# Kernel tuning notes

Measured on AMD Instinct MI355X. Metric: run time of the kernel, lower is better.

## Reference

```python
import jax, jax.numpy as jnp
import numpy as np

N, D, L = 4096, 256, 3
E = 1.0  # eye scale 'e'


def _adj(X, W, b):
    # AdjLearner_intra: two Linear+ELU layers, then dense similarity h @ h.T -> [N, N]
    h = jax.nn.elu(X @ W[0] + b[0])
    h = jax.nn.elu(h @ W[1] + b[1])
    return h @ h.T


def _mlp(x, W, b, bn):
    # GIN MLP: Linear -> BatchNorm1d (batch stats, training mode) -> ReLU -> Linear
    h = x @ W[0] + b[0]
    mu = h.mean(axis=0)
    var = h.var(axis=0)  # biased, matches torch BN training normalization
    h = (h - mu) * jax.lax.rsqrt(var + 1e-5) * bn[0] + bn[1]
    return jax.nn.relu(h) @ W[1] + b[1]


def _gin(X, aW, ab, mW, mb, mbn):
    I = jnp.eye(X.shape[0], dtype=X.dtype)
    acc = jnp.zeros_like(X)
    for i in range(L):  # fixed small layer count
        adj = _adj(X, aW, ab)
        oh = (adj > adj.mean()).astype(X.dtype)  # adj_onehot: threshold at global mean
        X = _mlp((oh + E * I) @ X, mW[i], mb[i], mbn[i])
        acc = acc + X
    return acc / L


def setup_inputs() -> dict:
    key = jax.random.key(0)
    ks = jax.random.split(key, 16)
    s = np.float32(1.0 / np.sqrt(D))
    d = {}
    for i, name in enumerate(["QV", "Q", "V", "A"]):
        d[name] = jax.random.normal(ks[i], (N, D), jnp.float32)
    for j, br in enumerate(["qv", "t", "v"]):
        k0, k1 = ks[4 + 2 * j], ks[5 + 2 * j]
        d[f"adjW_{br}"] = jax.random.normal(k0, (2, D, D), jnp.float32) * s
        d[f"adjb_{br}"] = jnp.zeros((2, D), jnp.float32)
        d[f"mlpW_{br}"] = jax.random.normal(k1, (L, 2, D, D), jnp.float32) * s
        d[f"mlpb_{br}"] = jnp.zeros((L, 2, D), jnp.float32)
        d[f"mlpbn_{br}"] = jnp.stack(
            [jnp.ones((L, D), jnp.float32), jnp.zeros((L, D), jnp.float32)], axis=1
        )  # [L, 2(gamma,beta), D]
    return d


def reference(QV, Q, V, A,
              adjW_qv, adjb_qv, mlpW_qv, mlpb_qv, mlpbn_qv,
              adjW_t, adjb_t, mlpW_t, mlpb_t, mlpbn_t,
              adjW_v, adjb_v, mlpW_v, mlpb_v, mlpbn_v):
    GQV = _gin(QV, adjW_qv, adjb_qv, mlpW_qv, mlpb_qv, mlpbn_qv)  # type=1
    GQ = _gin(Q, adjW_t, adjb_t, mlpW_t, mlpb_t, mlpbn_t)          # type=2
    GV = _gin(V, adjW_v, adjb_v, mlpW_v, mlpb_v, mlpbn_v)          # type=3
    GA = _gin(A, adjW_t, adjb_t, mlpW_t, mlpb_t, mlpbn_t)          # type=2 (shared with Q branch)
    mse = lambda a, b: jnp.mean((a - b) ** 2)
    return (mse(GQV, GA), mse(GQ, GA), mse(GV, GA))
```

## Files before the change

kernel.cpp:

```cpp
#include <hip/hip_runtime.h>
#include <hip/hip_bf16.h>
#include <stdint.h>

#define NN 4096
#define DD 256
#define NL 3
typedef unsigned int uint;
typedef unsigned short ushort_t;

typedef float f32x4 __attribute__((ext_vector_type(4)));
typedef short bf16x8 __attribute__((ext_vector_type(8)));

struct Ptrs4 { const float* p0; const float* p1; const float* p2; const float* p3; };
__device__ __forceinline__ const float* sel(const Ptrs4& p, int b) {
    return b == 0 ? p.p0 : b == 1 ? p.p1 : b == 2 ? p.p2 : p.p3;
}

__device__ __forceinline__ uint pkbf2(float a, float b) {
    __hip_bfloat162 t = __float22bfloat162_rn(float2{a, b});
    union { __hip_bfloat162 h; uint u; } c; c.h = t; return c.u;
}
__device__ __forceinline__ void split3_pk(float a, float b, uint& h, uint& m, uint& l) {
    h = pkbf2(a, b);
    float ha = __uint_as_float(h << 16), hb = __uint_as_float(h & 0xFFFF0000u);
    float ra = a - ha, rb = b - hb;
    m = pkbf2(ra, rb);
    float ma = __uint_as_float(m << 16), mb = __uint_as_float(m & 0xFFFF0000u);
    l = pkbf2(ra - ma, rb - mb);
}

typedef __attribute__((address_space(3))) uint lds_u32;
typedef __attribute__((address_space(1))) const uint glb_u32;
__device__ __forceinline__ void gload16(void* l, const void* g) {
    __builtin_amdgcn_global_load_lds((glb_u32*)g, (lds_u32*)l, 16, 0, 0);
}
__device__ __forceinline__ void gload4(void* l, const void* g) {
    __builtin_amdgcn_global_load_lds((glb_u32*)g, (lds_u32*)l, 4, 0, 0);
}

template<int MODE>
__global__ __launch_bounds__(256, 4)
void gemm_small(const float* __restrict__ Xin, Ptrs4 Wp, Ptrs4 bp,
                float* __restrict__ Out, float* __restrict__ cs, float* __restrict__ csq,
                ushort_t* __restrict__ Hso)
{
    const int b = blockIdx.z;
    const float* Wb = sel(Wp, b);
    const float* bb = sel(bp, b);
    const float* X = Xin + (size_t)b * NN * DD;
    float* O = Out + (size_t)b * NN * DD;
    ushort_t* HsO = Hso + (size_t)b * 3 * (size_t)DD * NN;
    const int row0 = blockIdx.y * 128, col0 = blockIdx.x * 64;
    const int tid = threadIdx.x;
    __shared__ float Asm[16][132];
    __shared__ float Bsm[16][68];
    const int tr = (tid >> 4) << 3, tc = (tid & 15) << 2;
    const int m = tid & 127, kk = (tid >> 7) << 3;
    const int bk = tid >> 4, bn = (tid & 15) << 2;
    const float* aSrc = X + (size_t)(row0 + m) * DD + kk;
    const float* bSrc = Wb + (size_t)bk * DD + col0 + bn;

    float acc[8][4] = {};
    float4 pa0 = *(const float4*)(aSrc);
    float4 pa1 = *(const float4*)(aSrc + 4);
    float4 pb  = *(const float4*)(bSrc);
    for (int t = 0; t < DD / 16; ++t) {
        Asm[kk+0][m]=pa0.x; Asm[kk+1][m]=pa0.y; Asm[kk+2][m]=pa0.z; Asm[kk+3][m]=pa0.w;
        Asm[kk+4][m]=pa1.x; Asm[kk+5][m]=pa1.y; Asm[kk+6][m]=pa1.z; Asm[kk+7][m]=pa1.w;
        *(float4*)&Bsm[bk][bn] = pb;
        __syncthreads();
        if (t < DD / 16 - 1) {
            const int k0 = (t + 1) * 16;
            pa0 = *(const float4*)(aSrc + k0);
            pa1 = *(const float4*)(aSrc + k0 + 4);
            pb  = *(const float4*)(bSrc + (size_t)k0 * DD);
        }
        #pragma unroll
        for (int k = 0; k < 16; ++k) {
            float a[8], bv[4];
            *(float4*)&a[0] = *(const float4*)&Asm[k][tr];
            *(float4*)&a[4] = *(const float4*)&Asm[k][tr + 4];
            *(float4*)&bv[0] = *(const float4*)&Bsm[k][tc];
            #pragma unroll
            for (int i = 0; i < 8; ++i)
                #pragma unroll
                for (int j = 0; j < 4; ++j)
                    acc[i][j] = fmaf(a[i], bv[j], acc[i][j]);
        }
        __syncthreads();
    }
    float bias4[4];
    *(float4*)bias4 = *(const float4*)(bb + col0 + tc);
    float s4[4] = {0.f,0.f,0.f,0.f}, q4[4] = {0.f,0.f,0.f,0.f};
    const int dph = col0 + tc;
    const size_t sb3 = (size_t)(dph >> 3) * (NN * 8) + (dph & 4);
    #pragma unroll
    for (int i = 0; i < 8; ++i) {
        float ov[4];
        #pragma unroll
        for (int j = 0; j < 4; ++j) {
            float v = acc[i][j] + bias4[j];
            if (MODE == 0 || MODE == 1 || MODE == 3) v = (v > 0.f) ? v : (expf(v) - 1.f);
            ov[j] = v;
            if (MODE == 1 || MODE == 3) s4[j] += v;
            if (MODE == 2) { s4[j] += v; q4[j] += v * v; }
        }
        if (MODE == 3) {
            uint2 vh, vm, vl;
            split3_pk(ov[0], ov[1], vh.x, vm.x, vl.x);
            split3_pk(ov[2], ov[3], vh.y, vm.y, vl.y);
            size_t off = sb3 + (size_t)(row0 + tr + i) * 8;
            *(uint2*)(HsO + off) = vh;
            *(uint2*)(HsO + (size_t)DD * NN + off) = vm;
            *(uint2*)(HsO + (size_t)2 * DD * NN + off) = vl;
        } else {
            float4 o; o.x = ov[0]; o.y = ov[1]; o.z = ov[2]; o.w = ov[3];
            *(float4*)(O + (size_t)(row0 + tr + i) * DD + col0 + tc) = o;
        }
    }
    if (MODE == 1 || MODE == 2 || MODE == 3) {
        __syncthreads();
        const int rg = tid >> 4;
        #pragma unroll
        for (int j = 0; j < 4; ++j) {
            Asm[rg][tc + j] = s4[j];
            if (MODE == 2) Bsm[rg][tc + j] = q4[j];
        }
        __syncthreads();
        if (tid < 64) {
            float s = 0.f, q = 0.f;
            #pragma unroll
            for (int r = 0; r < 16; ++r) { s += Asm[r][tid]; if (MODE == 2) q += Bsm[r][tid]; }
            atomicAdd(&cs[b * DD + col0 + tid], s);
            if (MODE == 2) atomicAdd(&csq[b * DD + col0 + tid], q);
        }
    }
}

__global__ void thresh_k(const float* __restrict__ cs, float* __restrict__ tvals)
{
    const int b = blockIdx.x, t = threadIdx.x;
    __shared__ float red[256];
    float v = cs[b * DD + t];
    red[t] = v * v;
    __syncthreads();
    for (int s = 128; s > 0; s >>= 1) { if (t < s) red[t] += red[t + s]; __syncthreads(); }
    if (t == 0) tvals[b] = red[0] * (1.0f / 16777216.0f);
}

__global__ __launch_bounds__(256)
void tsplit_x(const float* __restrict__ Xin, ushort_t* __restrict__ Sh,
              ushort_t* __restrict__ Sm, ushort_t* __restrict__ Sl)
{
    const int b = blockIdx.z;
    const int n0 = blockIdx.x * 64, d0 = blockIdx.y * 64;
    const float* X = Xin + (size_t)b * NN * DD;
    __shared__ float ls[64][65];
    const int tid = threadIdx.x;
    #pragma unroll
    for (int i = 0; i < 4; ++i) {
        int u = (i << 8) + tid;
        int r = u >> 4, c4 = (u & 15) << 2;
        float4 v = *(const float4*)(X + (size_t)(n0 + r) * DD + d0 + c4);
        ls[r][c4] = v.x; ls[r][c4+1] = v.y; ls[r][c4+2] = v.z; ls[r][c4+3] = v.w;
    }
    __syncthreads();
    const int d = tid >> 2, seg = (tid & 3) << 4;
    uint ph[8], pm[8], pl[8];
    #pragma unroll
    for (int jj = 0; jj < 8; ++jj) {
        float a = ls[seg + 2 * jj][d];
        float c = ls[seg + 2 * jj + 1][d];
        split3_pk(a, c, ph[jj], pm[jj], pl[jj]);
    }
    size_t idx = ((size_t)(b * DD + d0 + d)) * NN + n0 + seg;
    *(uint4*)(Sh + idx)     = *(uint4*)&ph[0];
    *(uint4*)(Sh + idx + 8) = *(uint4*)&ph[4];
    *(uint4*)(Sm + idx)     = *(uint4*)&pm[0];
    *(uint4*)(Sm + idx + 8) = *(uint4*)&pm[4];
    *(uint4*)(Sl + idx)     = *(uint4*)&pl[0];
    *(uint4*)(Sl + idx + 8) = *(uint4*)&pl[4];
}

__global__ __launch_bounds__(256, 3)
void adj_mfma_s(const float* __restrict__ H, const float* __restrict__ tvals,
                uint8_t* __restrict__ mask)
{
    int t = blockIdx.x;
    int by = 0, rem = 32;
    while (t >= rem) { t -= rem; rem--; by++; }
    const int bx = by + t;
    const int b = blockIdx.z;
    const int row0 = by * 128, col0 = bx * 128;
    const int tid = threadIdx.x;
    const int wave = tid >> 6, ln = tid & 15, quad = (tid >> 4) & 3;
    const int wrow = wave >> 1, wcol = wave & 1;
    const float* Hb = H + (size_t)b * NN * DD;
    uint8_t* Mb = mask + (size_t)b * NN * (NN / 8);
    __shared__ ushort_t hs[2][3][128][34];

    f32x4 acc[4][4] = {};
    for (int k0 = 0; k0 < DD; k0 += 32) {
        #pragma unroll
        for (int i = 0; i < 8; ++i) {
            int f = (i << 8) + tid;
            int sr = f >> 3;
            int side = sr >> 7, r = sr & 127, part = f & 7;
            int grow = (side ? col0 : row0) + r;
            float4 v = *(const float4*)(Hb + (size_t)grow * DD + k0 + part * 4);
            uint h0, m0, l0, h1, m1, l1;
            split3_pk(v.x, v.y, h0, m0, l0);
            split3_pk(v.z, v.w, h1, m1, l1);
            uint2 ph; ph.x = h0; ph.y = h1;
            uint2 pm; pm.x = m0; pm.y = m1;
            uint2 pl; pl.x = l0; pl.y = l1;
            *(uint2*)&hs[side][0][r][part * 4] = ph;
            *(uint2*)&hs[side][1][r][part * 4] = pm;
            *(uint2*)&hs[side][2][r][part * 4] = pl;
        }
        __syncthreads();
        bf16x8 af[4][3];
        #pragma unroll
        for (int mt = 0; mt < 4; ++mt)
            #pragma unroll
            for (int lvl = 0; lvl < 3; ++lvl)
                af[mt][lvl] = *(const bf16x8*)&hs[0][lvl][wrow * 64 + mt * 16 + ln][quad * 8];
        #pragma unroll
        for (int nt = 0; nt < 4; ++nt) {
            int n = wcol * 64 + nt * 16 + ln;
            bf16x8 bh = *(const bf16x8*)&hs[1][0][n][quad * 8];
            bf16x8 bm = *(const bf16x8*)&hs[1][1][n][quad * 8];
            bf16x8 bl = *(const bf16x8*)&hs[1][2][n][quad * 8];
            #pragma unroll
            for (int mt = 0; mt < 4; ++mt) {
                f32x4 a = acc[mt][nt];
                a = __builtin_amdgcn_mfma_f32_16x16x32_bf16(af[mt][0], bh, a, 0, 0, 0);
                a = __builtin_amdgcn_mfma_f32_16x16x32_bf16(af[mt][0], bm, a, 0, 0, 0);
                a = __builtin_amdgcn_mfma_f32_16x16x32_bf16(af[mt][1], bh, a, 0, 0, 0);
                a = __builtin_amdgcn_mfma_f32_16x16x32_bf16(af[mt][0], bl, a, 0, 0, 0);
                a = __builtin_amdgcn_mfma_f32_16x16x32_bf16(af[mt][2], bh, a, 0, 0, 0);
                a = __builtin_amdgcn_mfma_f32_16x16x32_bf16(af[mt][1], bm, a, 0, 0, 0);
                acc[mt][nt] = a;
            }
        }
        __syncthreads();
    }
    const float t2 = tvals[b];
    #pragma unroll
    for (int mt = 0; mt < 4; ++mt)
        #pragma unroll
        for (int nt = 0; nt < 4; ++nt) {
            bool p0 = acc[mt][nt][0] > t2, p1 = acc[mt][nt][1] > t2;
            bool p2 = acc[mt][nt][2] > t2, p3 = acc[mt][nt][3] > t2;
            unsigned long long bal[4];
            bal[0] = __ballot(p0); bal[1] = __ballot(p1);
            bal[2] = __ballot(p2); bal[3] = __ballot(p3);
            if ((tid & 63) < 16) {
                int q = ln >> 2, rsel = ln & 3;
                unsigned long long bv = rsel == 0 ? bal[0] : rsel == 1 ? bal[1]
                                       : rsel == 2 ? bal[2] : bal[3];
                ushort_t u16 = (ushort_t)((bv >> (q * 16)) & 0xFFFFull);
                int row = row0 + wrow * 64 + mt * 16 + ln;
                int colb = (col0 + wcol * 64 + nt * 16) >> 3;
                *(ushort_t*)(Mb + (size_t)row * (NN / 8) + colb) = u16;
            }
            uint nib = (p0 ? 1u : 0u) | (p1 ? 2u : 0u) | (p2 ? 4u : 0u) | (p3 ? 8u : 0u);
            uint other = (uint)__shfl_xor((int)nib, 16);
            if ((quad & 1) == 0) {
                uint byt = nib | (other << 4);
                int rowm = col0 + wcol * 64 + nt * 16 + ln;
                int colbm = ((row0 + wrow * 64 + mt * 16) >> 3) + (quad >> 1);
                Mb[(size_t)rowm * (NN / 8) + colbm] = (uint8_t)byt;
            }
        }
}

__global__ __launch_bounds__(256, 3)
void adj_mfma_v2(const ushort_t* __restrict__ Hs, const float* __restrict__ tvals,
                 uint8_t* __restrict__ mask)
{
    int t = blockIdx.x;
    int by = 0, rem = 32;
    while (t >= rem) { t -= rem; rem--; by++; }
    const int bx = by + t;
    const int b = blockIdx.z;
    const int row0 = by * 128, col0 = bx * 128;
    const int tid = threadIdx.x;
    const int wave = tid >> 6, ln = tid & 15, quad = (tid >> 4) & 3;
    const int wrow = wave >> 1, wcol = wave & 1;
    const ushort_t* Hb = Hs + (size_t)b * 3 * (size_t)DD * NN;
    uint8_t* Mb = mask + (size_t)b * NN * (NN / 8);
    __shared__ ushort_t hs2[6][4][128][8];

    const int grow = tid & 127;
    const int qb = tid >> 7;
    const size_t var0 = (size_t)qb * (NN * 8) + (size_t)(row0 + grow) * 8;
    const size_t var1 = (size_t)qb * (NN * 8) + (size_t)(col0 + grow) * 8;

    f32x4 acc[4][4] = {};
    for (int kb0 = 0; kb0 < DD / 8; kb0 += 4) {
        #pragma unroll
        for (int c = 0; c < 12; ++c) {
            const int sl = c >> 1, part = c & 1;
            const int side = sl / 3, lvl = sl % 3;
            const ushort_t* g = Hb + (size_t)lvl * DD * NN
                                   + (size_t)(kb0 + part * 2) * (NN * 8)
                                   + (side ? var1 : var0);
            char* l = (char*)&hs2[0][0][0][0] + (((sl * 8 + part * 4 + wave)) << 10);
            gload16(l, g);
        }
        __syncthreads();
        bf16x8 af[4][3];
        #pragma unroll
        for (int mt = 0; mt < 4; ++mt)
            #pragma unroll
            for (int lvl = 0; lvl < 3; ++lvl)
                af[mt][lvl] = *(const bf16x8*)&hs2[lvl][quad][wrow * 64 + mt * 16 + ln][0];
        #pragma unroll
        for (int nt = 0; nt < 4; ++nt) {
            const int n = wcol * 64 + nt * 16 + ln;
            bf16x8 bh = *(const bf16x8*)&hs2[3][quad][n][0];
            bf16x8 bm = *(const bf16x8*)&hs2[4][quad][n][0];
            bf16x8 bl = *(const bf16x8*)&hs2[5][quad][n][0];
            #pragma unroll
            for (int mt = 0; mt < 4; ++mt) {
                f32x4 a = acc[mt][nt];
                a = __builtin_amdgcn_mfma_f32_16x16x32_bf16(af[mt][0], bh, a, 0, 0, 0);
                a = __builtin_amdgcn_mfma_f32_16x16x32_bf16(af[mt][0], bm, a, 0, 0, 0);
                a = __builtin_amdgcn_mfma_f32_16x16x32_bf16(af[mt][1], bh, a, 0, 0, 0);
                a = __builtin_amdgcn_mfma_f32_16x16x32_bf16(af[mt][0], bl, a, 0, 0, 0);
                a = __builtin_amdgcn_mfma_f32_16x16x32_bf16(af[mt][2], bh, a, 0, 0, 0);
                a = __builtin_amdgcn_mfma_f32_16x16x32_bf16(af[mt][1], bm, a, 0, 0, 0);
                acc[mt][nt] = a;
            }
        }
        __syncthreads();
    }
    const float t2 = tvals[b];
    #pragma unroll
    for (int mt = 0; mt < 4; ++mt)
        #pragma unroll
        for (int nt = 0; nt < 4; ++nt) {
            bool p0 = acc[mt][nt][0] > t2, p1 = acc[mt][nt][1] > t2;
            bool p2 = acc[mt][nt][2] > t2, p3 = acc[mt][nt][3] > t2;
            unsigned long long bal[4];
            bal[0] = __ballot(p0); bal[1] = __ballot(p1);
            bal[2] = __ballot(p2); bal[3] = __ballot(p3);
            if ((tid & 63) < 16) {
                int q = ln >> 2, rsel = ln & 3;
                unsigned long long bv = rsel == 0 ? bal[0] : rsel == 1 ? bal[1]
                                       : rsel == 2 ? bal[2] : bal[3];
                ushort_t u16 = (ushort_t)((bv >> (q * 16)) & 0xFFFFull);
                int row = row0 + wrow * 64 + mt * 16 + ln;
                int colb = (col0 + wcol * 64 + nt * 16) >> 3;
                *(ushort_t*)(Mb + (size_t)row * (NN / 8) + colb) = u16;
            }
            uint nib = (p0 ? 1u : 0u) | (p1 ? 2u : 0u) | (p2 ? 4u : 0u) | (p3 ? 8u : 0u);
            uint other = (uint)__shfl_xor((int)nib, 16);
            if ((quad & 1) == 0) {
                uint byt = nib | (other << 4);
                int rowm = col0 + wcol * 64 + nt * 16 + ln;
                int colbm = ((row0 + wrow * 64 + mt * 16) >> 3) + (quad >> 1);
                Mb[(size_t)rowm * (NN / 8) + colbm] = (uint8_t)byt;
            }
        }
}

__global__ __launch_bounds__(256)
void masked_mfma(float* __restrict__ Xio, const ushort_t* __restrict__ Sh,
                 const ushort_t* __restrict__ Sm, const ushort_t* __restrict__ Sl,
                 const uint8_t* __restrict__ mask)
{
    const int b = blockIdx.z;
    const int row0 = blockIdx.y * 128, col0 = blockIdx.x * 64;
    const int tid = threadIdx.x;
    const int wave = tid >> 6, ln = tid & 15, quad = (tid >> 4) & 3;
    const int wrow = wave >> 1, wcol = wave & 1;
    float* X = Xio + (size_t)b * NN * DD;
    const size_t sb = (size_t)b * DD * NN;
    const ushort_t* Ss[3] = { Sh + sb, Sm + sb, Sl + sb };
    const uint* Mw = (const uint*)(mask + (size_t)b * NN * (NN / 8));
    __shared__ ushort_t bt2[2][3][2][64][32];
    __shared__ uint msk2[2][2][128];
    __shared__ uint lut[256][4];

    #pragma unroll
    for (int p = 0; p < 4; ++p)
        lut[tid][p] = (((tid >> (2 * p)) & 1u) ? 0x3F80u : 0u) |
                      (((tid >> (2 * p + 1)) & 1u) ? 0x3F800000u : 0u);

    const int c = tid >> 2;
    const int qp = (tid & 3) ^ ((tid >> 3) & 3);
    const size_t goff = (size_t)(col0 + c) * NN + (size_t)qp * 8;
    const size_t mrow = (size_t)(row0 + (tid & 127)) * 128;

    f32x4 acc[4][2] = {};

    #define STAGE(buf, t)                                                         \
        {                                                                         \
            const size_t j_ = (size_t)(t) * 64;                                   \
            _Pragma("unroll")                                                     \
            for (int lvl = 0; lvl < 3; ++lvl) {                                   \
                gload16((char*)&bt2[buf][lvl][0][0][0] + (wave << 10),            \
                        Ss[lvl] + goff + j_);                                     \
                gload16((char*)&bt2[buf][lvl][1][0][0] + (wave << 10),            \
                        Ss[lvl] + goff + j_ + 32);                                \
            }                                                                     \
            if (tid < 128) {                                                      \
                gload4((char*)&msk2[buf][0][0] + (wave << 8), Mw + mrow + 2*(t)); \
                gload4((char*)&msk2[buf][1][0] + (wave << 8), Mw + mrow + 2*(t)+1);\
            }                                                                     \
        }

    STAGE(0, 0);
    __syncthreads();

    for (int t = 0; t < NN / 64; ++t) {
        const int cur = t & 1;
        if (t < NN / 64 - 1) STAGE(cur ^ 1, t + 1);
        #pragma unroll
        for (int kk = 0; kk < 2; ++kk) {
            bf16x8 afr[4];
            #pragma unroll
            for (int mt = 0; mt < 4; ++mt) {
                uint w = msk2[cur][kk][wrow * 64 + mt * 16 + ln];
                uint byte = (w >> (quad * 8)) & 0xFFu;
                afr[mt] = *(const bf16x8*)&lut[byte][0];
            }
            #pragma unroll
            for (int nt = 0; nt < 2; ++nt) {
                const int n = wcol * 32 + nt * 16 + ln;
                const int slot = (quad ^ ((n >> 1) & 3)) * 8;
                bf16x8 bh = *(const bf16x8*)&bt2[cur][0][kk][n][slot];
                bf16x8 bm = *(const bf16x8*)&bt2[cur][1][kk][n][slot];
                bf16x8 bl = *(const bf16x8*)&bt2[cur][2][kk][n][slot];
                #pragma unroll
                for (int mt = 0; mt < 4; ++mt) {
                    f32x4 a = acc[mt][nt];
                    a = __builtin_amdgcn_mfma_f32_16x16x32_bf16(afr[mt], bh, a, 0, 0, 0);
                    a = __builtin_amdgcn_mfma_f32_16x16x32_bf16(afr[mt], bm, a, 0, 0, 0);
                    a = __builtin_amdgcn_mfma_f32_16x16x32_bf16(afr[mt], bl, a, 0, 0, 0);
                    acc[mt][nt] = a;
                }
            }
        }
        __syncthreads();
    }
    #undef STAGE
    #pragma unroll
    for (int mt = 0; mt < 4; ++mt)
        #pragma unroll
        for (int nt = 0; nt < 2; ++nt)
            #pragma unroll
            for (int r = 0; r < 4; ++r) {
                int row = row0 + wrow * 64 + mt * 16 + quad * 4 + r;
                int col = col0 + wcol * 32 + nt * 16 + ln;
                size_t idx = (size_t)row * DD + col;
                X[idx] = X[idx] + acc[mt][nt][r];
            }
}

__global__ __launch_bounds__(256, 4)
void gemm_bnrelu(const float* __restrict__ G, Ptrs4 Wp, Ptrs4 bp, Ptrs4 gbp,
                 const float* __restrict__ bns, const float* __restrict__ bnq,
                 float* __restrict__ Xout, float* __restrict__ accb, int first)
{
    const int b = blockIdx.z;
    const float* Wb = sel(Wp, b);
    const float* bb = sel(bp, b);
    const float* gb = sel(gbp, b);
    const float* Gb = G + (size_t)b * NN * DD;
    float* O = Xout + (size_t)b * NN * DD;
    float* Ab = accb + (size_t)b * NN * DD;
    const int row0 = blockIdx.y * 128, col0 = blockIdx.x * 64;
    const int tid = threadIdx.x;
    __shared__ float Asm[16][132];
    __shared__ float Bsm[16][68];
    __shared__ float scs[DD], shs[DD];
    {
        float mu = bns[b * DD + tid] * (1.0f / NN);
        float ms = bnq[b * DD + tid] * (1.0f / NN);
        float var = ms - mu * mu;
        float sc = gb[tid] / sqrtf(var + 1e-5f);
        scs[tid] = sc;
        shs[tid] = gb[DD + tid] - mu * sc;
    }
    __syncthreads();
    const int tr = (tid >> 4) << 3, tc = (tid & 15) << 2;
    const int m = tid & 127, kk = (tid >> 7) << 3;
    const int bk = tid >> 4, bn = (tid & 15) << 2;
    const float* aSrc = Gb + (size_t)(row0 + m) * DD + kk;
    const float* bSrc = Wb + (size_t)bk * DD + col0 + bn;

    float acc[8][4] = {};
    float4 pa0 = *(const float4*)(aSrc);
    float4 pa1 = *(const float4*)(aSrc + 4);
    float4 pb  = *(const float4*)(bSrc);
    for (int t = 0; t < DD / 16; ++t) {
        {
            const int kg = t * 16 + kk;
            float vv[8] = {pa0.x, pa0.y, pa0.z, pa0.w, pa1.x, pa1.y, pa1.z, pa1.w};
            #pragma unroll
            for (int i = 0; i < 8; ++i) {
                float v = fmaf(vv[i], scs[kg + i], shs[kg + i]);
                Asm[kk + i][m] = v > 0.f ? v : 0.f;
            }
            *(float4*)&Bsm[bk][bn] = pb;
        }
        __syncthreads();
        if (t < DD / 16 - 1) {
            const int k0 = (t + 1) * 16;
            pa0 = *(const float4*)(aSrc + k0);
            pa1 = *(const float4*)(aSrc + k0 + 4);
            pb  = *(const float4*)(bSrc + (size_t)k0 * DD);
        }
        #pragma unroll
        for (int k = 0; k < 16; ++k) {
            float a[8], bv[4];
            *(float4*)&a[0] = *(const float4*)&Asm[k][tr];
            *(float4*)&a[4] = *(const float4*)&Asm[k][tr + 4];
            *(float4*)&bv[0] = *(const float4*)&Bsm[k][tc];
            #pragma unroll
            for (int i = 0; i < 8; ++i)
                #pragma unroll
                for (int j = 0; j < 4; ++j)
                    acc[i][j] = fmaf(a[i], bv[j], acc[i][j]);
        }
        __syncthreads();
    }
    float bias4[4];
    *(float4*)bias4 = *(const float4*)(bb + col0 + tc);
    #pragma unroll
    for (int i = 0; i < 8; ++i) {
        size_t idx = (size_t)(row0 + tr + i) * DD + col0 + tc;
        float4 o;
        o.x = acc[i][0] + bias4[0]; o.y = acc[i][1] + bias4[1];
        o.z = acc[i][2] + bias4[2]; o.w = acc[i][3] + bias4[3];
        *(float4*)(O + idx) = o;
        if (first) {
            *(float4*)(Ab + idx) = o;
        } else {
            float4 p = *(const float4*)(Ab + idx);
            p.x += o.x; p.y += o.y; p.z += o.z; p.w += o.w;
            *(float4*)(Ab + idx) = p;
        }
    }
}

__global__ __launch_bounds__(256)
void mse_partial(const float* __restrict__ accb, double* __restrict__ msep)
{
    const int pair = blockIdx.x;
    const float* A_ = accb + (size_t)pair * NN * DD;
    const float* B_ = accb + (size_t)3 * NN * DD;
    const size_t total = (size_t)NN * DD;
    double s = 0.0;
    for (size_t i = (size_t)blockIdx.y * blockDim.x + threadIdx.x; i < total;
         i += (size_t)gridDim.y * blockDim.x) {
        float d = A_[i] - B_[i];
        s += (double)d * (double)d;
    }
    __shared__ double red[256];
    red[threadIdx.x] = s;
    __syncthreads();
    for (int st = 128; st > 0; st >>= 1) {
        if (threadIdx.x < st) red[threadIdx.x] += red[threadIdx.x + st];
        __syncthreads();
    }
    if (threadIdx.x == 0) atomicAdd(&msep[pair], red[0]);
}

__global__ void mse_final(const double* __restrict__ msep, float* __restrict__ out)
{
    int i = threadIdx.x;
    if (i < 3) out[i] = (float)(msep[i] / ((double)NN * DD) / 9.0);
}

static inline Ptrs4 mk4(const float* a, const float* b, const float* c, const float* d) {
    Ptrs4 p; p.p0 = a; p.p1 = b; p.p2 = c; p.p3 = d; return p;
}

extern "C" void kernel_launch(void* const* d_in, const int* in_sizes, int n_in,
                              void* d_out, int out_size, void* d_ws, size_t ws_size,
                              hipStream_t stream)
{
    (void)in_sizes; (void)n_in; (void)out_size;
    const float* adjW[3]  = {(const float*)d_in[4],  (const float*)d_in[9],  (const float*)d_in[14]};
    const float* adjb[3]  = {(const float*)d_in[5],  (const float*)d_in[10], (const float*)d_in[15]};
    const float* mlpW[3]  = {(const float*)d_in[6],  (const float*)d_in[11], (const float*)d_in[16]};
    const float* mlpb[3]  = {(const float*)d_in[7],  (const float*)d_in[12], (const float*)d_in[17]};
    const float* mlpbn[3] = {(const float*)d_in[8],  (const float*)d_in[13], (const float*)d_in[18]};

    char* ws = (char*)d_ws;
    double* msep  = (double*)ws;
    float* colsum = (float*)(ws + 64);
    float* bnsum  = colsum + 3 * 4 * DD;
    float* bnsq   = bnsum  + 3 * 4 * DD;
    float* tvals  = bnsq   + 3 * 4 * DD;
    const size_t tensN = (size_t)4 * NN * DD;
    const size_t HS_BYTES = (size_t)4 * 3 * DD * NN * 2;
    const size_t MASK_BYTES = (size_t)4 * NN * (NN / 8);

    float* Xbuf = (float*)(ws + 65536);
    float* Abuf = Xbuf + tensN;

    const size_t need_fast = 65536 + 2 * tensN * 4 + HS_BYTES + tensN * 4 + MASK_BYTES;
    const bool fast = ws_size >= need_fast;

    float* Bbuf = nullptr; float* accb; uint8_t* mask;
    ushort_t *Sh, *Sm, *Sl, *HsG = nullptr;
    if (fast) {
        char* hr = (char*)(Abuf + tensN);
        HsG  = (ushort_t*)hr;
        Sl   = (ushort_t*)hr;
        accb = (float*)(hr + HS_BYTES);
        mask = (uint8_t*)(accb + tensN);
    } else {
        Bbuf = Abuf + tensN;
        accb = Bbuf + tensN;
        mask = (uint8_t*)(accb + tensN);
        Sl   = (ushort_t*)Bbuf;
    }
    Sh = (ushort_t*)Abuf;
    Sm = Sh + tensN;

    hipMemsetAsync(ws, 0, 64 + 3 * 3 * 4 * DD * sizeof(float), stream);
    for (int b = 0; b < 4; ++b)
        hipMemcpyAsync(Xbuf + (size_t)b * NN * DD, d_in[b], (size_t)NN * DD * sizeof(float),
                       hipMemcpyDeviceToDevice, stream);

    dim3 gS(4, 32, 4);
    dim3 gA(528, 1, 4);
    dim3 gT(64, 4, 4);
    dim3 blk(256);

    for (int l = 0; l < NL; ++l) {
        float* cs_l = colsum + l * 4 * DD;
        float* bs_l = bnsum + l * 4 * DD;
        float* bq_l = bnsq  + l * 4 * DD;
        #define MK(arr, off) mk4(arr[0] + (off), arr[1] + (off), arr[2] + (off), arr[1] + (off))
        gemm_small<0><<<gS, blk, 0, stream>>>(Xbuf, MK(adjW, 0), MK(adjb, 0), Abuf,
                                              nullptr, nullptr, (ushort_t*)nullptr);
        if (fast) {
            gemm_small<3><<<gS, blk, 0, stream>>>(Abuf, MK(adjW, (size_t)DD * DD), MK(adjb, DD),
                                                  nullptr, cs_l, nullptr, HsG);
            thresh_k<<<4, blk, 0, stream>>>(cs_l, tvals);
            adj_mfma_v2<<<gA, blk, 0, stream>>>(HsG, tvals, mask);
        } else {
            gemm_small<1><<<gS, blk, 0, stream>>>(Abuf, MK(adjW, (size_t)DD * DD), MK(adjb, DD),
                                                  Bbuf, cs_l, nullptr, (ushort_t*)nullptr);
            thresh_k<<<4, blk, 0, stream>>>(cs_l, tvals);
            adj_mfma_s<<<gA, blk, 0, stream>>>(Bbuf, tvals, mask);
        }
        tsplit_x<<<gT, blk, 0, stream>>>(Xbuf, Sh, Sm, Sl);
        masked_mfma<<<gS, blk, 0, stream>>>(Xbuf, Sh, Sm, Sl, mask);
        const size_t w0 = (size_t)l * 2 * DD * DD, b0 = (size_t)l * 2 * DD;
        gemm_small<2><<<gS, blk, 0, stream>>>(Xbuf, MK(mlpW, w0), MK(mlpb, b0), Abuf,
                                              bs_l, bq_l, (ushort_t*)nullptr);
        gemm_bnrelu<<<gS, blk, 0, stream>>>(Abuf, MK(mlpW, w0 + (size_t)DD * DD), MK(mlpb, b0 + DD),
                                            MK(mlpbn, b0), bs_l, bq_l, Xbuf, accb, (l == 0) ? 1 : 0);
        #undef MK
    }
    mse_partial<<<dim3(3, 64), blk, 0, stream>>>(accb, msep);
    mse_final<<<1, 64, 0, stream>>>(msep, (float*)d_out);
}
```

Baseline: 1.164 ms.

## Run the small feature GEMMs on MFMA with a 3-way bf16 split of pre-split weights

Adds a one-time kernel that splits every adjacency and MLP weight matrix into transposed hi/mid/lo bf16 planes in workspace. Adds MFMA-based replacements for the first adjacency linear, the first MLP linear (with BN statistics) and the BN+ReLU second linear. These split activations on the fly and emulate fp32 accuracy with six bf16 MFMAs per tile. The goal is to move these DxD GEMMs off the fp32 vector ALU; the cost is extra split work, extra workspace, and a dependence on workspace being large enough.

```diff
diff --git a/kernel.cpp b/kernel.cpp
--- a/kernel.cpp
+++ b/kernel.cpp
@@ -15,6 +15,12 @@
 __device__ __forceinline__ const float* sel(const Ptrs4& p, int b) {
     return b == 0 ? p.p0 : b == 1 ? p.p1 : b == 2 ? p.p2 : p.p3;
 }
+struct Ptrs4U { const ushort_t* p0; const ushort_t* p1; const ushort_t* p2; const ushort_t* p3; };
+__device__ __forceinline__ const ushort_t* selU(const Ptrs4U& p, int b) {
+    return b == 0 ? p.p0 : b == 1 ? p.p1 : b == 2 ? p.p2 : p.p3;
+}
+struct PtrsW { const float* a0; const float* a1; const float* a2;
+               const float* m0; const float* m1; const float* m2; };
 
 __device__ __forceinline__ uint pkbf2(float a, float b) {
     __hip_bfloat162 t = __float22bfloat162_rn(float2{a, b});
@@ -135,6 +141,308 @@
             if (MODE == 2) atomicAdd(&csq[b * DD + col0 + tid], q);
         }
     }
+}
+
+__global__ __launch_bounds__(256)
+void wsplitk(PtrsW W, ushort_t* __restrict__ Wsp)
+{
+    const int z = blockIdx.z;
+    const float* src;
+    if (z < 6) {
+        const float* base = (z >> 1) == 0 ? W.a0 : (z >> 1) == 1 ? W.a1 : W.a2;
+        src = base + (size_t)(z & 1) * DD * DD;
+    } else {
+        int zz = z - 6;
+        const float* base = (zz / 6) == 0 ? W.m0 : (zz / 6) == 1 ? W.m1 : W.m2;
+        src = base + (size_t)(zz % 6) * DD * DD;
+    }
+    ushort_t* dst = Wsp + (size_t)z * 3 * DD * DD;
+    const int k0 = blockIdx.x * 64, c0 = blockIdx.y * 64;
+    __shared__ float ls[64][65];
+    const int tid = threadIdx.x;
+    #pragma unroll
+    for (int i = 0; i < 4; ++i) {
+        int u = (i << 8) + tid;
+        int r = u >> 4, c4 = (u & 15) << 2;
+        float4 v = *(const float4*)(src + (size_t)(k0 + r) * DD + c0 + c4);
+        ls[r][c4] = v.x; ls[r][c4+1] = v.y; ls[r][c4+2] = v.z; ls[r][c4+3] = v.w;
+    }
+    __syncthreads();
+    const int col = tid >> 2, seg = (tid & 3) << 4;
+    uint ph[8], pm[8], pl[8];
+    #pragma unroll
+    for (int jj = 0; jj < 8; ++jj) {
+        float a = ls[seg + 2 * jj][col];
+        float c = ls[seg + 2 * jj + 1][col];
+        split3_pk(a, c, ph[jj], pm[jj], pl[jj]);
+    }
+    size_t idx = (size_t)(c0 + col) * DD + k0 + seg;
+    #pragma unroll
+    for (int lvl = 0; lvl < 3; ++lvl) {
+        uint* pp = lvl == 0 ? ph : lvl == 1 ? pm : pl;
+        *(uint4*)(dst + (size_t)lvl * DD * DD + idx)     = *(uint4*)&pp[0];
+        *(uint4*)(dst + (size_t)lvl * DD * DD + idx + 8) = *(uint4*)&pp[4];
+    }
+}
+
+template<int MODE>
+__global__ void gemm_mfma(const float* __restrict__ Xin, Ptrs4U Wsp, Ptrs4 bp,
+                          float* __restrict__ Out, float* __restrict__ cs,
+                          float* __restrict__ csq)
+{
+    const int b = blockIdx.z;
+    const ushort_t* Wb = selU(Wsp, b);
+    const float* bb = sel(bp, b);
+    const float* X = Xin + (size_t)b * NN * DD;
+    float* O = Out + (size_t)b * NN * DD;
+    const int row0 = blockIdx.y * 128, col0 = blockIdx.x * 64;
+    const int tid = threadIdx.x;
+    const int wave = tid >> 6, ln = tid & 15, quad = (tid >> 4) & 3;
+    const int wrow = wave >> 1, wcol = wave & 1;
+    __shared__ ushort_t As[3][128][32];
+    __shared__ ushort_t Bs[2][3][64][32];
+
+    const int arow = tid >> 1, kb16 = (tid & 1) << 4;
+    const int xr = (arow >> 1) & 3;
+    const int s0 = (((kb16 >> 3) + 0) ^ xr) << 3;
+    const int s1 = (((kb16 >> 3) + 1) ^ xr) << 3;
+    const float* aSrc = X + (size_t)(row0 + arow) * DD + kb16;
+
+    const int qp = (tid & 3) ^ ((tid >> 3) & 3);
+    const size_t bgoff = (size_t)(col0 + (tid >> 2)) * DD + (size_t)qp * 8;
+
+    #define BSTAGE(buf, t_) { \
+        _Pragma("unroll") \
+        for (int lvl = 0; lvl < 3; ++lvl) \
+            gload16((char*)&Bs[buf][lvl][0][0] + (wave << 10), \
+                    Wb + (size_t)lvl * DD * DD + bgoff + (size_t)(t_) * 32); }
+
+    f32x4 acc[4][2] = {};
+    float4 pa0 = *(const float4*)(aSrc),     pa1 = *(const float4*)(aSrc + 4);
+    float4 pa2 = *(const float4*)(aSrc + 8), pa3 = *(const float4*)(aSrc + 12);
+    BSTAGE(0, 0)
+    for (int t = 0; t < DD / 32; ++t) {
+        {
+            uint hh[8], mm[8], ll[8];
+            split3_pk(pa0.x, pa0.y, hh[0], mm[0], ll[0]);
+            split3_pk(pa0.z, pa0.w, hh[1], mm[1], ll[1]);
+            split3_pk(pa1.x, pa1.y, hh[2], mm[2], ll[2]);
+            split3_pk(pa1.z, pa1.w, hh[3], mm[3], ll[3]);
+            split3_pk(pa2.x, pa2.y, hh[4], mm[4], ll[4]);
+            split3_pk(pa2.z, pa2.w, hh[5], mm[5], ll[5]);
+            split3_pk(pa3.x, pa3.y, hh[6], mm[6], ll[6]);
+            split3_pk(pa3.z, pa3.w, hh[7], mm[7], ll[7]);
+            uint4 v;
+            v.x=hh[0]; v.y=hh[1]; v.z=hh[2]; v.w=hh[3]; *(uint4*)&As[0][arow][s0] = v;
+            v.x=hh[4]; v.y=hh[5]; v.z=hh[6]; v.w=hh[7]; *(uint4*)&As[0][arow][s1] = v;
+            v.x=mm[0]; v.y=mm[1]; v.z=mm[2]; v.w=mm[3]; *(uint4*)&As[1][arow][s0] = v;
+            v.x=mm[4]; v.y=mm[5]; v.z=mm[6]; v.w=mm[7]; *(uint4*)&As[1][arow][s1] = v;
+            v.x=ll[0]; v.y=ll[1]; v.z=ll[2]; v.w=ll[3]; *(uint4*)&As[2][arow][s0] = v;
+            v.x=ll[4]; v.y=ll[5]; v.z=ll[6]; v.w=ll[7]; *(uint4*)&As[2][arow][s1] = v;
+        }
+        __syncthreads();
+        if (t < DD / 32 - 1) {
+            const float* an = aSrc + (t + 1) * 32;
+            pa0 = *(const float4*)(an);     pa1 = *(const float4*)(an + 4);
+            pa2 = *(const float4*)(an + 8); pa3 = *(const float4*)(an + 12);
+            BSTAGE((t + 1) & 1, t + 1)
+        }
+        bf16x8 af[4][3];
+        #pragma unroll
+        for (int mt = 0; mt < 4; ++mt) {
+            const int row = wrow * 64 + mt * 16 + ln;
+            const int sl = ((quad ^ ((row >> 1) & 3)) << 3);
+            #pragma unroll
+            for (int lvl = 0; lvl < 3; ++lvl)
+                af[mt][lvl] = *(const bf16x8*)&As[lvl][row][sl];
+        }
+        const int cur = t & 1;
+        #pragma unroll
+        for (int nt = 0; nt < 2; ++nt) {
+            const int n = wcol * 32 + nt * 16 + ln;
+            const int slot = ((quad ^ ((n >> 1) & 3)) << 3);
+            bf16x8 bh = *(const bf16x8*)&Bs[cur][0][n][slot];
+            bf16x8 bm = *(const bf16x8*)&Bs[cur][1][n][slot];
+            bf16x8 bl = *(const bf16x8*)&Bs[cur][2][n][slot];
+            #pragma unroll
+            for (int mt = 0; mt < 4; ++mt) {
+                f32x4 a = acc[mt][nt];
+                a = __builtin_amdgcn_mfma_f32_16x16x32_bf16(af[mt][0], bh, a, 0, 0, 0);
+                a = __builtin_amdgcn_mfma_f32_16x16x32_bf16(af[mt][0], bm, a, 0, 0, 0);
+                a = __builtin_amdgcn_mfma_f32_16x16x32_bf16(af[mt][1], bh, a, 0, 0, 0);
+                a = __builtin_amdgcn_mfma_f32_16x16x32_bf16(af[mt][0], bl, a, 0, 0, 0);
+                a = __builtin_amdgcn_mfma_f32_16x16x32_bf16(af[mt][2], bh, a, 0, 0, 0);
+                a = __builtin_amdgcn_mfma_f32_16x16x32_bf16(af[mt][1], bm, a, 0, 0, 0);
+                acc[mt][nt] = a;
+            }
+        }
+        __syncthreads();
+    }
+    #undef BSTAGE
+
+    float bcol[2], ssum[2] = {0.f, 0.f}, qsum[2] = {0.f, 0.f};
+    #pragma unroll
+    for (int nt = 0; nt < 2; ++nt) bcol[nt] = bb[col0 + wcol * 32 + nt * 16 + ln];
+    #pragma unroll
+    for (int mt = 0; mt < 4; ++mt)
+        #pragma unroll
+        for (int nt = 0; nt < 2; ++nt)
+            #pragma unroll
+            for (int r = 0; r < 4; ++r) {
+                int row = row0 + wrow * 64 + mt * 16 + quad * 4 + r;
+                int col = col0 + wcol * 32 + nt * 16 + ln;
+                float v = acc[mt][nt][r] + bcol[nt];
+                if (MODE == 0) v = (v > 0.f) ? v : (expf(v) - 1.f);
+                if (MODE == 2) { ssum[nt] += v; qsum[nt] += v * v; }
+                O[(size_t)row * DD + col] = v;
+            }
+    if (MODE == 2) {
+        float* scrS = (float*)&As[0][0][0];
+        float* scrQ = scrS + 512;
+        const int rg = wrow * 4 + quad;
+        #pragma unroll
+        for (int nt = 0; nt < 2; ++nt) {
+            const int cl = wcol * 32 + nt * 16 + ln;
+            scrS[rg * 64 + cl] = ssum[nt];
+            scrQ[rg * 64 + cl] = qsum[nt];
+        }
+        __syncthreads();
+        if (tid < 64) {
+            float s = 0.f, q = 0.f;
+            #pragma unroll
+            for (int r = 0; r < 8; ++r) { s += scrS[r * 64 + tid]; q += scrQ[r * 64 + tid]; }
+            atomicAdd(&cs[b * DD + col0 + tid], s);
+            atomicAdd(&csq[b * DD + col0 + tid], q);
+        }
+    }
+}
+
+__global__ void gemm_bnrelu_m(const float* __restrict__ G, Ptrs4U Wsp, Ptrs4 bp, Ptrs4 gbp,
+                              const float* __restrict__ bns, const float* __restrict__ bnq,
+                              float* __restrict__ Xout, float* __restrict__ accb, int first)
+{
+    const int b = blockIdx.z;
+    const ushort_t* Wb = selU(Wsp, b);
+    const float* bb = sel(bp, b);
+    const float* gb = sel(gbp, b);
+    const float* Gb = G + (size_t)b * NN * DD;
+    float* O = Xout + (size_t)b * NN * DD;
+    float* Ab = accb + (size_t)b * NN * DD;
+    const int row0 = blockIdx.y * 128, col0 = blockIdx.x * 64;
+    const int tid = threadIdx.x;
+    const int wave = tid >> 6, ln = tid & 15, quad = (tid >> 4) & 3;
+    const int wrow = wave >> 1, wcol = wave & 1;
+    __shared__ ushort_t As[3][128][32];
+    __shared__ ushort_t Bs[2][3][64][32];
+    __shared__ float scs[DD], shs[DD];
+    {
+        float mu = bns[b * DD + tid] * (1.0f / NN);
+        float ms = bnq[b * DD + tid] * (1.0f / NN);
+        float var = ms - mu * mu;
+        float sc = gb[tid] / sqrtf(var + 1e-5f);
+        scs[tid] = sc;
+        shs[tid] = gb[DD + tid] - mu * sc;
+    }
+
+    const int arow = tid >> 1, kb16 = (tid & 1) << 4;
+    const int xr = (arow >> 1) & 3;
+    const int s0 = (((kb16 >> 3) + 0) ^ xr) << 3;
+    const int s1 = (((kb16 >> 3) + 1) ^ xr) << 3;
+    const float* aSrc = Gb + (size_t)(row0 + arow) * DD + kb16;
+
+    const int qp = (tid & 3) ^ ((tid >> 3) & 3);
+    const size_t bgoff = (size_t)(col0 + (tid >> 2)) * DD + (size_t)qp * 8;
+
+    #define BSTAGE(buf, t_) { \
+        _Pragma("unroll") \
+        for (int lvl = 0; lvl < 3; ++lvl) \
+            gload16((char*)&Bs[buf][lvl][0][0] + (wave << 10), \
+                    Wb + (size_t)lvl * DD * DD + bgoff + (size_t)(t_) * 32); }
+
+    f32x4 acc[4][2] = {};
+    float4 pa0 = *(const float4*)(aSrc),     pa1 = *(const float4*)(aSrc + 4);
+    float4 pa2 = *(const float4*)(aSrc + 8), pa3 = *(const float4*)(aSrc + 12);
+    BSTAGE(0, 0)
+    __syncthreads();
+    for (int t = 0; t < DD / 32; ++t) {
+        {
+            const int kg = t * 32 + kb16;
+            float f[16] = {pa0.x,pa0.y,pa0.z,pa0.w, pa1.x,pa1.y,pa1.z,pa1.w,
+                           pa2.x,pa2.y,pa2.z,pa2.w, pa3.x,pa3.y,pa3.z,pa3.w};
+            #pragma unroll
+            for (int i = 0; i < 16; ++i) {
+                float v = fmaf(f[i], scs[kg + i], shs[kg + i]);
+                f[i] = v > 0.f ? v : 0.f;
+            }
+            uint hh[8], mm[8], ll[8];
+            #pragma unroll
+            for (int p = 0; p < 8; ++p)
+                split3_pk(f[2 * p], f[2 * p + 1], hh[p], mm[p], ll[p]);
+            uint4 v;
+            v.x=hh[0]; v.y=hh[1]; v.z=hh[2]; v.w=hh[3]; *(uint4*)&As[0][arow][s0] = v;
+            v.x=hh[4]; v.y=hh[5]; v.z=hh[6]; v.w=hh[7]; *(uint4*)&As[0][arow][s1] = v;
+            v.x=mm[0]; v.y=mm[1]; v.z=mm[2]; v.w=mm[3]; *(uint4*)&As[1][arow][s0] = v;
+            v.x=mm[4]; v.y=mm[5]; v.z=mm[6]; v.w=mm[7]; *(uint4*)&As[1][arow][s1] = v;
+            v.x=ll[0]; v.y=ll[1]; v.z=ll[2]; v.w=ll[3]; *(uint4*)&As[2][arow][s0] = v;
+            v.x=ll[4]; v.y=ll[5]; v.z=ll[6]; v.w=ll[7]; *(uint4*)&As[2][arow][s1] = v;
+        }
+        __syncthreads();
+        if (t < DD / 32 - 1) {
+            const float* an = aSrc + (t + 1) * 32;
+            pa0 = *(const float4*)(an);     pa1 = *(const float4*)(an + 4);
+            pa2 = *(const float4*)(an + 8); pa3 = *(const float4*)(an + 12);
+            BSTAGE((t + 1) & 1, t + 1)
+        }
+        bf16x8 af[4][3];
+        #pragma unroll
+        for (int mt = 0; mt < 4; ++mt) {
+            const int row = wrow * 64 + mt * 16 + ln;
+            const int sl = ((quad ^ ((row >> 1) & 3)) << 3);
+            #pragma unroll
+            for (int lvl = 0; lvl < 3; ++lvl)
+                af[mt][lvl] = *(const bf16x8*)&As[lvl][row][sl];
+        }
+        const int cur = t & 1;
+        #pragma unroll
+        for (int nt = 0; nt < 2; ++nt) {
+            const int n = wcol * 32 + nt * 16 + ln;
+            const int slot = ((quad ^ ((n >> 1) & 3)) << 3);
+            bf16x8 bh = *(const bf16x8*)&Bs[cur][0][n][slot];
+            bf16x8 bm = *(const bf16x8*)&Bs[cur][1][n][slot];
+            bf16x8 bl = *(const bf16x8*)&Bs[cur][2][n][slot];
+            #pragma unroll
+            for (int mt = 0; mt < 4; ++mt) {
+                f32x4 a = acc[mt][nt];
+                a = __builtin_amdgcn_mfma_f32_16x16x32_bf16(af[mt][0], bh, a, 0, 0, 0);
+                a = __builtin_amdgcn_mfma_f32_16x16x32_bf16(af[mt][0], bm, a, 0, 0, 0);
+                a = __builtin_amdgcn_mfma_f32_16x16x32_bf16(af[mt][1], bh, a, 0, 0, 0);
+                a = __builtin_amdgcn_mfma_f32_16x16x32_bf16(af[mt][0], bl, a, 0, 0, 0);
+                a = __builtin_amdgcn_mfma_f32_16x16x32_bf16(af[mt][2], bh, a, 0, 0, 0);
+                a = __builtin_amdgcn_mfma_f32_16x16x32_bf16(af[mt][1], bm, a, 0, 0, 0);
+                acc[mt][nt] = a;
+            }
+        }
+        __syncthreads();
+    }
+    #undef BSTAGE
+
+    float bcol[2];
+    #pragma unroll
+    for (int nt = 0; nt < 2; ++nt) bcol[nt] = bb[col0 + wcol * 32 + nt * 16 + ln];
+    #pragma unroll
+    for (int mt = 0; mt < 4; ++mt)
+        #pragma unroll
+        for (int nt = 0; nt < 2; ++nt)
+            #pragma unroll
+            for (int r = 0; r < 4; ++r) {
+                int row = row0 + wrow * 64 + mt * 16 + quad * 4 + r;
+                int col = col0 + wcol * 32 + nt * 16 + ln;
+                size_t idx = (size_t)row * DD + col;
+                float v = acc[mt][nt][r] + bcol[nt];
+                O[idx] = v;
+                if (first) Ab[idx] = v;
+                else       Ab[idx] = Ab[idx] + v;
+            }
 }
 
 __global__ void thresh_k(const float* __restrict__ cs, float* __restrict__ tvals)
@@ -579,6 +887,9 @@
 static inline Ptrs4 mk4(const float* a, const float* b, const float* c, const float* d) {
     Ptrs4 p; p.p0 = a; p.p1 = b; p.p2 = c; p.p3 = d; return p;
 }
+static inline Ptrs4U mk4u(const ushort_t* a, const ushort_t* b, const ushort_t* c, const ushort_t* d) {
+    Ptrs4U p; p.p0 = a; p.p1 = b; p.p2 = c; p.p3 = d; return p;
+}
 
 extern "C" void kernel_launch(void* const* d_in, const int* in_sizes, int n_in,
                               void* d_out, int out_size, void* d_ws, size_t ws_size,
@@ -600,21 +911,24 @@
     const size_t tensN = (size_t)4 * NN * DD;
     const size_t HS_BYTES = (size_t)4 * 3 * DD * NN * 2;
     const size_t MASK_BYTES = (size_t)4 * NN * (NN / 8);
+    const size_t WSP_BYTES = (size_t)24 * 3 * DD * DD * 2;
 
     float* Xbuf = (float*)(ws + 65536);
     float* Abuf = Xbuf + tensN;
 
     const size_t need_fast = 65536 + 2 * tensN * 4 + HS_BYTES + tensN * 4 + MASK_BYTES;
-    const bool fast = ws_size >= need_fast;
+    const bool fast  = ws_size >= need_fast;
+    const bool fast2 = ws_size >= need_fast + WSP_BYTES;
 
     float* Bbuf = nullptr; float* accb; uint8_t* mask;
-    ushort_t *Sh, *Sm, *Sl, *HsG = nullptr;
+    ushort_t *Sh, *Sm, *Sl, *HsG = nullptr, *Wsp = nullptr;
     if (fast) {
         char* hr = (char*)(Abuf + tensN);
         HsG  = (ushort_t*)hr;
         Sl   = (ushort_t*)hr;
         accb = (float*)(hr + HS_BYTES);
         mask = (uint8_t*)(accb + tensN);
+        Wsp  = (ushort_t*)(mask + MASK_BYTES);
     } else {
         Bbuf = Abuf + tensN;
         accb = Bbuf + tensN;
@@ -634,13 +948,27 @@
     dim3 gT(64, 4, 4);
     dim3 blk(256);
 
+    if (fast2) {
+        PtrsW wp; wp.a0 = adjW[0]; wp.a1 = adjW[1]; wp.a2 = adjW[2];
+                  wp.m0 = mlpW[0]; wp.m1 = mlpW[1]; wp.m2 = mlpW[2];
+        wsplitk<<<dim3(4, 4, 24), blk, 0, stream>>>(wp, Wsp);
+    }
+    const size_t MATB = (size_t)3 * DD * DD;
+    #define WMATA(s)    (Wsp + (size_t)0 * MATB)
     for (int l = 0; l < NL; ++l) {
         float* cs_l = colsum + l * 4 * DD;
         float* bs_l = bnsum + l * 4 * DD;
         float* bq_l = bnsq  + l * 4 * DD;
         #define MK(arr, off) mk4(arr[0] + (off), arr[1] + (off), arr[2] + (off), arr[1] + (off))
-        gemm_small<0><<<gS, blk, 0, stream>>>(Xbuf, MK(adjW, 0), MK(adjb, 0), Abuf,
-                                              nullptr, nullptr, (ushort_t*)nullptr);
+        #define MKW(expr0, expr1, expr2) mk4u(Wsp + (expr0) * MATB, Wsp + (expr1) * MATB, \
+                                              Wsp + (expr2) * MATB, Wsp + (expr1) * MATB)
+        if (fast2) {
+            gemm_mfma<0><<<gS, blk, 0, stream>>>(Xbuf, MKW(0, 2, 4), MK(adjb, 0),
+                                                 Abuf, nullptr, nullptr);
+        } else {
+            gemm_small<0><<<gS, blk, 0, stream>>>(Xbuf, MK(adjW, 0), MK(adjb, 0), Abuf,
+                                                  nullptr, nullptr, (ushort_t*)nullptr);
+        }
         if (fast) {
             gemm_small<3><<<gS, blk, 0, stream>>>(Abuf, MK(adjW, (size_t)DD * DD), MK(adjb, DD),
                                                   nullptr, cs_l, nullptr, HsG);
@@ -655,10 +983,21 @@
         tsplit_x<<<gT, blk, 0, stream>>>(Xbuf, Sh, Sm, Sl);
         masked_mfma<<<gS, blk, 0, stream>>>(Xbuf, Sh, Sm, Sl, mask);
         const size_t w0 = (size_t)l * 2 * DD * DD, b0 = (size_t)l * 2 * DD;
-        gemm_small<2><<<gS, blk, 0, stream>>>(Xbuf, MK(mlpW, w0), MK(mlpb, b0), Abuf,
-                                              bs_l, bq_l, (ushort_t*)nullptr);
-        gemm_bnrelu<<<gS, blk, 0, stream>>>(Abuf, MK(mlpW, w0 + (size_t)DD * DD), MK(mlpb, b0 + DD),
-                                            MK(mlpbn, b0), bs_l, bq_l, Xbuf, accb, (l == 0) ? 1 : 0);
+        if (fast2) {
+            gemm_mfma<2><<<gS, blk, 0, stream>>>(Xbuf,
+                MKW(6 + 0 * 6 + l * 2, 6 + 1 * 6 + l * 2, 6 + 2 * 6 + l * 2),
+                MK(mlpb, b0), Abuf, bs_l, bq_l);
+            gemm_bnrelu_m<<<gS, blk, 0, stream>>>(Abuf,
+                MKW(6 + 0 * 6 + l * 2 + 1, 6 + 1 * 6 + l * 2 + 1, 6 + 2 * 6 + l * 2 + 1),
+                MK(mlpb, b0 + DD), MK(mlpbn, b0), bs_l, bq_l, Xbuf, accb, (l == 0) ? 1 : 0);
+        } else {
+            gemm_small<2><<<gS, blk, 0, stream>>>(Xbuf, MK(mlpW, w0), MK(mlpb, b0), Abuf,
+                                                  bs_l, bq_l, (ushort_t*)nullptr);
+            gemm_bnrelu<<<gS, blk, 0, stream>>>(Abuf, MK(mlpW, w0 + (size_t)DD * DD),
+                                                MK(mlpb, b0 + DD), MK(mlpbn, b0),
+                                                bs_l, bq_l, Xbuf, accb, (l == 0) ? 1 : 0);
+        }
+        #undef MKW
         #undef MK
     }
     mse_partial<<<dim3(3, 64), blk, 0, stream>>>(accb, msep);
```

Result: faster. 1.005 ms (-13.6%).
